# Kernel optimization log

Measured on AMD Instinct MI355X. Metric: run time of the kernel, lower is better.

The kernel has to match this reference:

```python
import jax, jax.numpy as jnp
import numpy as np

HIDDEN = 1024
NUM_HEADS = 16
HEAD_DIM = HIDDEN // NUM_HEADS


def setup_inputs() -> dict:
    key = jax.random.key(0)
    ks = jax.random.split(key, 11)
    s = 1.0 / np.sqrt(HIDDEN)
    x = jax.random.normal(ks[0], (4, 2048, HIDDEN), dtype=jnp.float32)
    Wq = jax.random.uniform(ks[1], (HIDDEN, HIDDEN), jnp.float32, -s, s)
    bq = jax.random.uniform(ks[2], (HIDDEN,), jnp.float32, -s, s)
    Wk = jax.random.uniform(ks[3], (HIDDEN, HIDDEN), jnp.float32, -s, s)
    bk = jax.random.uniform(ks[4], (HIDDEN,), jnp.float32, -s, s)
    Wv = jax.random.uniform(ks[5], (HIDDEN, HIDDEN), jnp.float32, -s, s)
    bv = jax.random.uniform(ks[6], (HIDDEN,), jnp.float32, -s, s)
    Wo = jax.random.uniform(ks[7], (HIDDEN, HIDDEN), jnp.float32, -s, s)
    bo = jax.random.uniform(ks[8], (HIDDEN,), jnp.float32, -s, s)
    ln_g = jnp.ones((HIDDEN,), jnp.float32)
    ln_b = jnp.zeros((HIDDEN,), jnp.float32)
    return {"x": x, "Wq": Wq, "bq": bq, "Wk": Wk, "bk": bk,
            "Wv": Wv, "bv": bv, "Wo": Wo, "bo": bo,
            "ln_g": ln_g, "ln_b": ln_b}


def _layer_norm(x, g, b, eps=1e-5):
    mu = jnp.mean(x, axis=-1, keepdims=True)
    var = jnp.var(x, axis=-1, keepdims=True)
    return (x - mu) * jax.lax.rsqrt(var + eps) * g + b


def reference(x, Wq, bq, Wk, bk, Wv, bv, Wo, bo, ln_g, ln_b):
    B, S, _ = x.shape
    residual = x
    h = _layer_norm(x, ln_g, ln_b)
    # projections (torch Linear: y = h @ W.T + b)
    q = (h @ Wq.T + bq).reshape(B, S, NUM_HEADS, HEAD_DIM).transpose(0, 2, 1, 3)
    k = (h @ Wk.T + bk).reshape(B, S, NUM_HEADS, HEAD_DIM).transpose(0, 2, 1, 3)
    v = (h @ Wv.T + bv).reshape(B, S, NUM_HEADS, HEAD_DIM).transpose(0, 2, 1, 3)
    scores = jnp.einsum('bhqd,bhkd->bhqk', q, k) / np.sqrt(HEAD_DIM).astype(np.float32)
    weights = jax.nn.softmax(scores, axis=-1)  # dropout = identity (eval mode)
    context = jnp.einsum('bhqk,bhkd->bhqd', weights, v)
    context = context.transpose(0, 2, 1, 3).reshape(B, S, HIDDEN)
    out = context @ Wo.T + bo
    return out + residual
```

## Files before the change

### kernel.cpp

```cpp
#include <hip/hip_runtime.h>

typedef unsigned short u16;
typedef unsigned int   u32;
using bf16x8 = __attribute__((ext_vector_type(8))) __bf16;
using f32x4  = __attribute__((ext_vector_type(4))) float;
using u32x2  = __attribute__((ext_vector_type(2))) unsigned int;

__device__ __forceinline__ u16 f2b(float f){
  union { float f; u32 i; } v; v.f = f;
  u32 r = v.i + 0x7FFFu + ((v.i >> 16) & 1u);
  return (u16)(r >> 16);
}
__device__ __forceinline__ u32 pk_bf16_trunc(float a, float b){
  return __builtin_amdgcn_perm(__float_as_uint(b), __float_as_uint(a), 0x07060302u);
}

__global__ __launch_bounds__(256) void cvt_w(const float* __restrict__ s0, const float* __restrict__ s1,
                                             const float* __restrict__ s2, const float* __restrict__ s3,
                                             u16* __restrict__ d){
  const float* srcs[4] = {s0, s1, s2, s3};
  const float* s = srcs[blockIdx.y];
  u16* dd = d + (size_t)blockIdx.y * (1024u * 1024u);
  const int i = (blockIdx.x * 256 + threadIdx.x) * 4;
  float4 v = *(const float4*)(s + i);
  uint2 o;
  o.x = (u32)f2b(v.x) | ((u32)f2b(v.y) << 16);
  o.y = (u32)f2b(v.z) | ((u32)f2b(v.w) << 16);
  *(uint2*)(dd + i) = o;
}

__global__ __launch_bounds__(256) void ln_kernel(const float* __restrict__ x, const float* __restrict__ g,
                                                 const float* __restrict__ be, u16* __restrict__ h){
  const int row = blockIdx.x, tid = threadIdx.x;
  const float* xr = x + (size_t)row * 1024u;
  float4 raw = *(const float4*)(xr + tid * 4);
  float s  = raw.x + raw.y + raw.z + raw.w;
  float sq = raw.x*raw.x + raw.y*raw.y + raw.z*raw.z + raw.w*raw.w;
  #pragma unroll
  for (int m = 1; m < 64; m <<= 1){ s += __shfl_xor(s, m); sq += __shfl_xor(sq, m); }
  __shared__ float ws[4], wq[4];
  if ((tid & 63) == 0){ ws[tid >> 6] = s; wq[tid >> 6] = sq; }
  __syncthreads();
  s  = ws[0] + ws[1] + ws[2] + ws[3];
  sq = wq[0] + wq[1] + wq[2] + wq[3];
  const float mu = s * (1.0f / 1024.0f);
  const float rstd = rsqrtf(sq * (1.0f / 1024.0f) - mu * mu + 1e-5f);
  float4 gg = *(const float4*)(g + tid * 4);
  float4 bb = *(const float4*)(be + tid * 4);
  float y0 = (raw.x - mu) * rstd * gg.x + bb.x;
  float y1 = (raw.y - mu) * rstd * gg.y + bb.y;
  float y2 = (raw.z - mu) * rstd * gg.z + bb.z;
  float y3 = (raw.w - mu) * rstd * gg.w + bb.w;
  uint2 outv;
  outv.x = (u32)f2b(y0) | ((u32)f2b(y1) << 16);
  outv.y = (u32)f2b(y2) | ((u32)f2b(y3) << 16);
  *(uint2*)(h + (size_t)row * 1024u + tid * 4) = outv;
}

__global__ __launch_bounds__(256) void gemm_qkv(const u16* __restrict__ A, const u16* __restrict__ Wcat,
                                                const float* __restrict__ bq, const float* __restrict__ bk,
                                                const float* __restrict__ bv,
                                                u16* __restrict__ qo, u16* __restrict__ ko, u16* __restrict__ vt){
  __shared__ u16 lA[2][4096];
  __shared__ u16 lB[2][4096];
  const int tid = threadIdx.x;
  const int lane = tid & 63, wv = tid >> 6, l15 = lane & 15, quad = lane >> 4;
  const int wr = wv >> 1, wc = wv & 1;
  const int row0 = blockIdx.x * 128, col0 = blockIdx.y * 128;
  const int K = 1024;

  const int r0_ = tid >> 2,         c0_ = tid & 3;
  const int r1_ = (256 + tid) >> 2, c1_ = (256 + tid) & 3;
  const u16* Asrc0 = A    + (size_t)(row0 + r0_) * K + (c0_ ^ ((r0_ >> 1) & 3)) * 8;
  const u16* Asrc1 = A    + (size_t)(row0 + r1_) * K + (c1_ ^ ((r1_ >> 1) & 3)) * 8;
  const u16* Bsrc0 = Wcat + (size_t)(col0 + r0_) * K + (c0_ ^ ((r0_ >> 1) & 3)) * 8;
  const u16* Bsrc1 = Wcat + (size_t)(col0 + r1_) * K + (c1_ ^ ((r1_ >> 1) & 3)) * 8;
  const int cr = (quad ^ ((l15 >> 1) & 3)) * 8;

  f32x4 acc[4][4] = {};
  uint4 ar0, ar1, br0, br1;
  ar0 = *(const uint4*)(Asrc0);
  ar1 = *(const uint4*)(Asrc1);
  br0 = *(const uint4*)(Bsrc0);
  br1 = *(const uint4*)(Bsrc1);
  *(uint4*)&lA[0][tid * 8] = ar0;
  *(uint4*)&lA[0][(256 + tid) * 8] = ar1;
  *(uint4*)&lB[0][tid * 8] = br0;
  *(uint4*)&lB[0][(256 + tid) * 8] = br1;
  ar0 = *(const uint4*)(Asrc0 + 32);
  ar1 = *(const uint4*)(Asrc1 + 32);
  br0 = *(const uint4*)(Bsrc0 + 32);
  br1 = *(const uint4*)(Bsrc1 + 32);
  __syncthreads();

  for (int kt = 0; kt < 32; ++kt){
    const int cur = kt & 1;
    if (kt < 31){
      *(uint4*)&lA[cur ^ 1][tid * 8] = ar0;
      *(uint4*)&lA[cur ^ 1][(256 + tid) * 8] = ar1;
      *(uint4*)&lB[cur ^ 1][tid * 8] = br0;
      *(uint4*)&lB[cur ^ 1][(256 + tid) * 8] = br1;
    }
    if (kt < 30){
      const int o = (kt + 2) * 32;
      ar0 = *(const uint4*)(Asrc0 + o);
      ar1 = *(const uint4*)(Asrc1 + o);
      br0 = *(const uint4*)(Bsrc0 + o);
      br1 = *(const uint4*)(Bsrc1 + o);
    }
    bf16x8 af[4], bf[4];
    #pragma unroll
    for (int i = 0; i < 4; ++i) af[i] = *(const bf16x8*)&lA[cur][(wr * 64 + i * 16 + l15) * 32 + cr];
    #pragma unroll
    for (int j = 0; j < 4; ++j) bf[j] = *(const bf16x8*)&lB[cur][(wc * 64 + j * 16 + l15) * 32 + cr];
    #pragma unroll
    for (int i = 0; i < 4; ++i)
      #pragma unroll
      for (int j = 0; j < 4; ++j)
        acc[i][j] = __builtin_amdgcn_mfma_f32_16x16x32_bf16(af[i], bf[j], acc[i][j], 0, 0, 0);
    __syncthreads();
  }
  const int sel = col0 >> 10;
  if (sel < 2){
    const float* bias = (sel == 0) ? bq : bk;
    u16* dst = (sel == 0) ? qo : ko;
    #pragma unroll
    for (int i = 0; i < 4; ++i){
      const int grow = row0 + wr * 64 + i * 16 + quad * 4;
      #pragma unroll
      for (int j = 0; j < 4; ++j){
        const int gcol = (col0 & 1023) + wc * 64 + j * 16 + l15;
        const float bb = bias[gcol];
        #pragma unroll
        for (int r = 0; r < 4; ++r){
          size_t off = (size_t)(grow + r) * 1024u + gcol;
          dst[off] = f2b(acc[i][j][r] + bb);
        }
      }
    }
  } else {
    u16* pw = &lA[0][0] + wv * 2048;
    const int bglob = row0 >> 11;
    const int head  = ((col0 & 1023) >> 6) + wc;
    const int srem0 = (row0 & 2047) + wr * 64;
    const size_t vbase = (size_t)((bglob * 16 + head) * 64) * 2048u;
    #pragma unroll
    for (int p = 0; p < 2; ++p){
      #pragma unroll
      for (int i2 = 0; i2 < 2; ++i2){
        const int i = p * 2 + i2;
        #pragma unroll
        for (int j = 0; j < 4; ++j){
          const int d = j * 16 + l15;
          const float bv_ = bv[(col0 & 1023) + wc * 64 + d];
          const int u = (i2 * 4 + quad) ^ (d & 7);
          uint2 pk;
          pk.x = (u32)f2b(acc[i][j][0] + bv_) | ((u32)f2b(acc[i][j][1] + bv_) << 16);
          pk.y = (u32)f2b(acc[i][j][2] + bv_) | ((u32)f2b(acc[i][j][3] + bv_) << 16);
          *(uint2*)&pw[d * 32 + u * 4] = pk;
        }
      }
      const int dl = lane;
      #pragma unroll
      for (int c = 0; c < 4; ++c){
        const int u0 = (2 * c) ^ (dl & 7), u1 = (2 * c + 1) ^ (dl & 7);
        uint2 lo = *(const uint2*)&pw[dl * 32 + u0 * 4];
        uint2 hi = *(const uint2*)&pw[dl * 32 + u1 * 4];
        uint4 o4; o4.x = lo.x; o4.y = lo.y; o4.z = hi.x; o4.w = hi.y;
        *(uint4*)(vt + vbase + (size_t)dl * 2048u + srem0 + p * 32 + c * 8) = o4;
      }
    }
  }
}

__global__ __launch_bounds__(256) void gemm_out(const u16* __restrict__ A, const u16* __restrict__ W,
                                                const float* __restrict__ bias, const float* __restrict__ res,
                                                float* __restrict__ C, int M, int N, int K){
  __shared__ u16 lA[2][4096];
  __shared__ u16 lB[2][4096];
  const int tid = threadIdx.x;
  const int lane = tid & 63, wv = tid >> 6, l15 = lane & 15, quad = lane >> 4;
  const int wr = wv >> 1, wc = wv & 1;
  const int row0 = blockIdx.x * 128, col0 = blockIdx.y * 128;

  const int r0_ = tid >> 2,         c0_ = tid & 3;
  const int r1_ = (256 + tid) >> 2, c1_ = (256 + tid) & 3;
  const u16* Asrc0 = A + (size_t)(row0 + r0_) * K + (c0_ ^ ((r0_ >> 1) & 3)) * 8;
  const u16* Asrc1 = A + (size_t)(row0 + r1_) * K + (c1_ ^ ((r1_ >> 1) & 3)) * 8;
  const u16* Bsrc0 = W + (size_t)(col0 + r0_) * K + (c0_ ^ ((r0_ >> 1) & 3)) * 8;
  const u16* Bsrc1 = W + (size_t)(col0 + r1_) * K + (c1_ ^ ((r1_ >> 1) & 3)) * 8;
  const int cr = (quad ^ ((l15 >> 1) & 3)) * 8;

  f32x4 acc[4][4] = {};
  const int nkt = K >> 5;
  uint4 ar0, ar1, br0, br1;
  ar0 = *(const uint4*)(Asrc0);
  ar1 = *(const uint4*)(Asrc1);
  br0 = *(const uint4*)(Bsrc0);
  br1 = *(const uint4*)(Bsrc1);
  *(uint4*)&lA[0][tid * 8] = ar0;
  *(uint4*)&lA[0][(256 + tid) * 8] = ar1;
  *(uint4*)&lB[0][tid * 8] = br0;
  *(uint4*)&lB[0][(256 + tid) * 8] = br1;
  ar0 = *(const uint4*)(Asrc0 + 32);
  ar1 = *(const uint4*)(Asrc1 + 32);
  br0 = *(const uint4*)(Bsrc0 + 32);
  br1 = *(const uint4*)(Bsrc1 + 32);
  __syncthreads();

  for (int kt = 0; kt < nkt; ++kt){
    const int cur = kt & 1;
    if (kt < nkt - 1){
      *(uint4*)&lA[cur ^ 1][tid * 8] = ar0;
      *(uint4*)&lA[cur ^ 1][(256 + tid) * 8] = ar1;
      *(uint4*)&lB[cur ^ 1][tid * 8] = br0;
      *(uint4*)&lB[cur ^ 1][(256 + tid) * 8] = br1;
    }
    if (kt < nkt - 2){
      const int o = (kt + 2) * 32;
      ar0 = *(const uint4*)(Asrc0 + o);
      ar1 = *(const uint4*)(Asrc1 + o);
      br0 = *(const uint4*)(Bsrc0 + o);
      br1 = *(const uint4*)(Bsrc1 + o);
    }
    bf16x8 af[4], bf[4];
    #pragma unroll
    for (int i = 0; i < 4; ++i) af[i] = *(const bf16x8*)&lA[cur][(wr * 64 + i * 16 + l15) * 32 + cr];
    #pragma unroll
    for (int j = 0; j < 4; ++j) bf[j] = *(const bf16x8*)&lB[cur][(wc * 64 + j * 16 + l15) * 32 + cr];
    #pragma unroll
    for (int i = 0; i < 4; ++i)
      #pragma unroll
      for (int j = 0; j < 4; ++j)
        acc[i][j] = __builtin_amdgcn_mfma_f32_16x16x32_bf16(af[i], bf[j], acc[i][j], 0, 0, 0);
    __syncthreads();
  }
  #pragma unroll
  for (int i = 0; i < 4; ++i){
    const int grow = row0 + wr * 64 + i * 16 + quad * 4;
    #pragma unroll
    for (int j = 0; j < 4; ++j){
      const int gcol = col0 + wc * 64 + j * 16 + l15;
      const float bb = bias[gcol];
      #pragma unroll
      for (int r = 0; r < 4; ++r){
        size_t off = (size_t)(grow + r) * N + gcol;
        C[off] = acc[i][j][r] + bb + res[off];
      }
    }
  }
}

__global__ __launch_bounds__(256, 2) void attn_kernel(const u16* __restrict__ Q, const u16* __restrict__ K,
                                                      const u16* __restrict__ Vt, u16* __restrict__ O){
  __shared__ u16 kls[2][64 * 64];
  __shared__ u16 vls[2][64 * 64];
  const int tid = threadIdx.x;
  const int lane = tid & 63, wv = tid >> 6, l15 = lane & 15, quad = lane >> 4;
  const int bh = blockIdx.x & 63, qt = blockIdx.x >> 6;
  const int b = bh >> 4, hh = bh & 15;
  const int q0 = qt * 256;
  const u16* Qg = Q + ((size_t)b * 2048u) * 1024u + hh * 64;
  const u16* Kg = K + ((size_t)b * 2048u) * 1024u + hh * 64;
  const u16* Vg = Vt + (size_t)bh * 64u * 2048u;
  u16* Og = O + ((size_t)b * 2048u) * 1024u + hh * 64;

  const int sr = tid >> 3, sc = tid & 7, sr2 = sr + 32;
  const int sx = (sc ^ (sr & 7)) * 8;
  const int c0 = ((quad ^ (l15 & 7))) * 8;

  const float QSCALE = 0.125f * 1.44269504f;
  bf16x8 qf2[4][2];
  #pragma unroll
  for (int g = 0; g < 4; ++g)
    #pragma unroll
    for (int kk = 0; kk < 2; ++kk){
      qf2[g][kk] = *(const bf16x8*)(Qg + (size_t)(q0 + wv * 64 + g * 16 + l15) * 1024u + kk * 32 + quad * 8);
      #pragma unroll
      for (int e = 0; e < 8; ++e) qf2[g][kk][e] = (__bf16)((float)qf2[g][kk][e] * QSCALE);
    }

  bf16x8 ones_f;
  {
    const __bf16 onev = (__bf16)1.0f, zerov = (__bf16)0.0f;
    #pragma unroll
    for (int e = 0; e < 8; ++e) ones_f[e] = (l15 == 0) ? onev : zerov;
  }

  f32x4 o2[4][4] = {};
  f32x4 o_l[4] = {};
  const f32x4 zf = {0.f, 0.f, 0.f, 0.f};

  uint4 kr0, kr1, vr0, vr1;
  kr0 = *(const uint4*)(Kg + (size_t)sr  * 1024u + sc * 8);
  vr0 = *(const uint4*)(Vg + (size_t)sr  * 2048u + sc * 8);
  kr1 = *(const uint4*)(Kg + (size_t)sr2 * 1024u + sc * 8);
  vr1 = *(const uint4*)(Vg + (size_t)sr2 * 2048u + sc * 8);
  *(uint4*)&kls[0][sr  * 64 + sx] = kr0;
  *(uint4*)&vls[0][sr  * 64 + sx] = vr0;
  *(uint4*)&kls[0][sr2 * 64 + sx] = kr1;
  *(uint4*)&vls[0][sr2 * 64 + sx] = vr1;
  kr0 = *(const uint4*)(Kg + (size_t)(64 + sr)  * 1024u + sc * 8);
  vr0 = *(const uint4*)(Vg + (size_t)sr  * 2048u + 64 + sc * 8);
  kr1 = *(const uint4*)(Kg + (size_t)(64 + sr2) * 1024u + sc * 8);
  vr1 = *(const uint4*)(Vg + (size_t)sr2 * 2048u + 64 + sc * 8);
  __syncthreads();

  for (int kt = 0; kt < 32; ++kt){
    const int cur = kt & 1;
    const u16* kb = kls[cur];
    const u16* vb = vls[cur];
    if (kt < 31){
      u16* kw = kls[cur ^ 1];
      u16* vw = vls[cur ^ 1];
      *(uint4*)&kw[sr  * 64 + sx] = kr0;
      *(uint4*)&vw[sr  * 64 + sx] = vr0;
      *(uint4*)&kw[sr2 * 64 + sx] = kr1;
      *(uint4*)&vw[sr2 * 64 + sx] = vr1;
    }
    if (kt < 30){
      const int s0 = (kt + 2) * 64;
      kr0 = *(const uint4*)(Kg + (size_t)(s0 + sr)  * 1024u + sc * 8);
      vr0 = *(const uint4*)(Vg + (size_t)sr  * 2048u + s0 + sc * 8);
      kr1 = *(const uint4*)(Kg + (size_t)(s0 + sr2) * 1024u + sc * 8);
      vr1 = *(const uint4*)(Vg + (size_t)sr2 * 2048u + s0 + sc * 8);
    }

    f32x4 s2[4][4];
    #pragma unroll
    for (int j = 0; j < 4; ++j){
      const int rb = (j * 16 + l15) * 64;
      bf16x8 kfr0 = *(const bf16x8*)&kb[rb + c0];
      bf16x8 kfr1 = *(const bf16x8*)&kb[rb + (c0 ^ 32)];
      #pragma unroll
      for (int g = 0; g < 4; ++g){
        f32x4 a = __builtin_amdgcn_mfma_f32_16x16x32_bf16(kfr0, qf2[g][0], zf, 0, 0, 0);
        s2[g][j] = __builtin_amdgcn_mfma_f32_16x16x32_bf16(kfr1, qf2[g][1], a, 0, 0, 0);
      }
    }

    #pragma unroll
    for (int g = 0; g < 4; ++g)
      #pragma unroll
      for (int j = 0; j < 4; ++j)
        #pragma unroll
        for (int r = 0; r < 4; ++r)
          s2[g][j][r] = __builtin_amdgcn_exp2f(s2[g][j][r]);

    #pragma unroll
    for (int kk = 0; kk < 2; ++kk){
      bf16x8 afr[4];
      #pragma unroll
      for (int g = 0; g < 4; ++g){
        const int j0 = kk * 2, j1 = j0 + 1;
        u32 A0 = pk_bf16_trunc(s2[g][j0][0], s2[g][j0][1]);
        u32 A1 = pk_bf16_trunc(s2[g][j0][2], s2[g][j0][3]);
        u32 B0 = pk_bf16_trunc(s2[g][j1][0], s2[g][j1][1]);
        u32 B1 = pk_bf16_trunc(s2[g][j1][2], s2[g][j1][3]);
        u32x2 r1 = __builtin_amdgcn_permlane32_swap(A0, B0, false, false);
        u32x2 r2 = __builtin_amdgcn_permlane16_swap(r1[0], r1[1], false, false);
        u32x2 r3 = __builtin_amdgcn_permlane32_swap(A1, B1, false, false);
        u32x2 r4 = __builtin_amdgcn_permlane16_swap(r3[0], r3[1], false, false);
        union { uint4 u; bf16x8 v; } cv;
        cv.u.x = r2[0]; cv.u.y = r4[0]; cv.u.z = r2[1]; cv.u.w = r4[1];
        afr[g] = cv.v;
      }
      #pragma unroll
      for (int g = 0; g < 4; ++g)
        o_l[g] = __builtin_amdgcn_mfma_f32_16x16x32_bf16(afr[g], ones_f, o_l[g], 0, 0, 0);
      #pragma unroll
      for (int j2 = 0; j2 < 4; ++j2){
        bf16x8 bfr = *(const bf16x8*)&vb[(j2 * 16 + l15) * 64 + (c0 ^ (kk * 32))];
        #pragma unroll
        for (int g = 0; g < 4; ++g)
          o2[g][j2] = __builtin_amdgcn_mfma_f32_16x16x32_bf16(afr[g], bfr, o2[g][j2], 0, 0, 0);
      }
    }
    __syncthreads();
  }

  #pragma unroll
  for (int g = 0; g < 4; ++g){
    float lr[4];
    #pragma unroll
    for (int r = 0; r < 4; ++r) lr[r] = 1.0f / __shfl(o_l[g][r], quad * 16);
    #pragma unroll
    for (int j2 = 0; j2 < 4; ++j2){
      #pragma unroll
      for (int r = 0; r < 4; ++r){
        const int qrow = q0 + wv * 64 + g * 16 + quad * 4 + r;
        const int d = j2 * 16 + l15;
        Og[(size_t)qrow * 1024u + d] = f2b(o2[g][j2][r] * lr[r]);
      }
    }
  }
}

extern "C" void kernel_launch(void* const* d_in, const int* in_sizes, int n_in,
                              void* d_out, int out_size, void* d_ws, size_t ws_size,
                              hipStream_t stream){
  (void)in_sizes; (void)n_in; (void)out_size; (void)ws_size;
  const float* x   = (const float*)d_in[0];
  const float* Wq  = (const float*)d_in[1];
  const float* bq  = (const float*)d_in[2];
  const float* Wk  = (const float*)d_in[3];
  const float* bk  = (const float*)d_in[4];
  const float* Wv  = (const float*)d_in[5];
  const float* bv  = (const float*)d_in[6];
  const float* Wo  = (const float*)d_in[7];
  const float* bo  = (const float*)d_in[8];
  const float* lng = (const float*)d_in[9];
  const float* lnb = (const float*)d_in[10];
  float* out = (float*)d_out;

  const size_t TE = (size_t)8192 * 1024;
  u16* ws0 = (u16*)d_ws;
  u16* ws1 = ws0 + TE;
  u16* ws2 = ws1 + TE;
  u16* wsw = ws2 + TE;
  u16* wob = wsw + (size_t)3 * 1024 * 1024;
  u16* vt  = (u16*)d_out;

  cvt_w<<<dim3(1024, 4), 256, 0, stream>>>(Wq, Wk, Wv, Wo, wsw);
  ln_kernel<<<dim3(8192), 256, 0, stream>>>(x, lng, lnb, ws0);
  gemm_qkv<<<dim3(64, 24), 256, 0, stream>>>(ws0, wsw, bq, bk, bv, ws1, ws2, vt);
  attn_kernel<<<dim3(512), 256, 0, stream>>>(ws1, ws2, vt, ws1);
  gemm_out<<<dim3(64, 8), 256, 0, stream>>>(ws1, wob, bo, x, out, 8192, 1024, 1024);
}
```

Before: 267.0 us.

## Use direct global-to-LDS loads in QKV and output projection GEMMs

Replaces the register-staged global loads and LDS stores in both GEMM kernels with global_load_lds direct-to-LDS transfers. Synchronisation becomes manual vmcnt/lgkmcnt waits plus raw s_barrier. The aim is to free VGPRs and cut the LDS store instructions from the main loop. The prefetch distance drops from two tiles (one in registers, one in LDS) to one. Correctness now depends on the hand-written waitcnt counts and on the 16-byte LDS layout matching lane order.

```diff
diff --git a/kernel.cpp b/kernel.cpp
--- a/kernel.cpp
+++ b/kernel.cpp
@@ -14,6 +14,10 @@
 __device__ __forceinline__ u32 pk_bf16_trunc(float a, float b){
   return __builtin_amdgcn_perm(__float_as_uint(b), __float_as_uint(a), 0x07060302u);
 }
+
+#define GLL(gp, lp) __builtin_amdgcn_global_load_lds( \
+    (const __attribute__((address_space(1))) void*)(gp), \
+    (__attribute__((address_space(3))) void*)(lp), 16, 0, 0)
 
 __global__ __launch_bounds__(256) void cvt_w(const float* __restrict__ s0, const float* __restrict__ s1,
                                              const float* __restrict__ s2, const float* __restrict__ s3,
@@ -78,36 +82,25 @@
   const int cr = (quad ^ ((l15 >> 1) & 3)) * 8;
 
   f32x4 acc[4][4] = {};
-  uint4 ar0, ar1, br0, br1;
-  ar0 = *(const uint4*)(Asrc0);
-  ar1 = *(const uint4*)(Asrc1);
-  br0 = *(const uint4*)(Bsrc0);
-  br1 = *(const uint4*)(Bsrc1);
-  *(uint4*)&lA[0][tid * 8] = ar0;
-  *(uint4*)&lA[0][(256 + tid) * 8] = ar1;
-  *(uint4*)&lB[0][tid * 8] = br0;
-  *(uint4*)&lB[0][(256 + tid) * 8] = br1;
-  ar0 = *(const uint4*)(Asrc0 + 32);
-  ar1 = *(const uint4*)(Asrc1 + 32);
-  br0 = *(const uint4*)(Bsrc0 + 32);
-  br1 = *(const uint4*)(Bsrc1 + 32);
-  __syncthreads();
+
+  GLL(Asrc0, &lA[0][tid * 8]);
+  GLL(Asrc1, &lA[0][(256 + tid) * 8]);
+  GLL(Bsrc0, &lB[0][tid * 8]);
+  GLL(Bsrc1, &lB[0][(256 + tid) * 8]);
 
   for (int kt = 0; kt < 32; ++kt){
     const int cur = kt & 1;
     if (kt < 31){
-      *(uint4*)&lA[cur ^ 1][tid * 8] = ar0;
-      *(uint4*)&lA[cur ^ 1][(256 + tid) * 8] = ar1;
-      *(uint4*)&lB[cur ^ 1][tid * 8] = br0;
-      *(uint4*)&lB[cur ^ 1][(256 + tid) * 8] = br1;
-    }
-    if (kt < 30){
-      const int o = (kt + 2) * 32;
-      ar0 = *(const uint4*)(Asrc0 + o);
-      ar1 = *(const uint4*)(Asrc1 + o);
-      br0 = *(const uint4*)(Bsrc0 + o);
-      br1 = *(const uint4*)(Bsrc1 + o);
-    }
+      const int o = (kt + 1) * 32;
+      GLL(Asrc0 + o, &lA[cur ^ 1][tid * 8]);
+      GLL(Asrc1 + o, &lA[cur ^ 1][(256 + tid) * 8]);
+      GLL(Bsrc0 + o, &lB[cur ^ 1][tid * 8]);
+      GLL(Bsrc1 + o, &lB[cur ^ 1][(256 + tid) * 8]);
+      asm volatile("s_waitcnt vmcnt(4)" ::: "memory");
+    } else {
+      asm volatile("s_waitcnt vmcnt(0)" ::: "memory");
+    }
+    asm volatile("s_barrier" ::: "memory");
     bf16x8 af[4], bf[4];
     #pragma unroll
     for (int i = 0; i < 4; ++i) af[i] = *(const bf16x8*)&lA[cur][(wr * 64 + i * 16 + l15) * 32 + cr];
@@ -118,8 +111,11 @@
       #pragma unroll
       for (int j = 0; j < 4; ++j)
         acc[i][j] = __builtin_amdgcn_mfma_f32_16x16x32_bf16(af[i], bf[j], acc[i][j], 0, 0, 0);
-    __syncthreads();
-  }
+    asm volatile("s_waitcnt lgkmcnt(0)" ::: "memory");
+    __builtin_amdgcn_sched_barrier(0);
+    asm volatile("s_barrier" ::: "memory");
+  }
+
   const int sel = col0 >> 10;
   if (sel < 2){
     const float* bias = (sel == 0) ? bq : bk;
@@ -193,36 +189,25 @@
 
   f32x4 acc[4][4] = {};
   const int nkt = K >> 5;
-  uint4 ar0, ar1, br0, br1;
-  ar0 = *(const uint4*)(Asrc0);
-  ar1 = *(const uint4*)(Asrc1);
-  br0 = *(const uint4*)(Bsrc0);
-  br1 = *(const uint4*)(Bsrc1);
-  *(uint4*)&lA[0][tid * 8] = ar0;
-  *(uint4*)&lA[0][(256 + tid) * 8] = ar1;
-  *(uint4*)&lB[0][tid * 8] = br0;
-  *(uint4*)&lB[0][(256 + tid) * 8] = br1;
-  ar0 = *(const uint4*)(Asrc0 + 32);
-  ar1 = *(const uint4*)(Asrc1 + 32);
-  br0 = *(const uint4*)(Bsrc0 + 32);
-  br1 = *(const uint4*)(Bsrc1 + 32);
-  __syncthreads();
+
+  GLL(Asrc0, &lA[0][tid * 8]);
+  GLL(Asrc1, &lA[0][(256 + tid) * 8]);
+  GLL(Bsrc0, &lB[0][tid * 8]);
+  GLL(Bsrc1, &lB[0][(256 + tid) * 8]);
 
   for (int kt = 0; kt < nkt; ++kt){
     const int cur = kt & 1;
     if (kt < nkt - 1){
-      *(uint4*)&lA[cur ^ 1][tid * 8] = ar0;
-      *(uint4*)&lA[cur ^ 1][(256 + tid) * 8] = ar1;
-      *(uint4*)&lB[cur ^ 1][tid * 8] = br0;
-      *(uint4*)&lB[cur ^ 1][(256 + tid) * 8] = br1;
-    }
-    if (kt < nkt - 2){
-      const int o = (kt + 2) * 32;
-      ar0 = *(const uint4*)(Asrc0 + o);
-      ar1 = *(const uint4*)(Asrc1 + o);
-      br0 = *(const uint4*)(Bsrc0 + o);
-      br1 = *(const uint4*)(Bsrc1 + o);
-    }
+      const int o = (kt + 1) * 32;
+      GLL(Asrc0 + o, &lA[cur ^ 1][tid * 8]);
+      GLL(Asrc1 + o, &lA[cur ^ 1][(256 + tid) * 8]);
+      GLL(Bsrc0 + o, &lB[cur ^ 1][tid * 8]);
+      GLL(Bsrc1 + o, &lB[cur ^ 1][(256 + tid) * 8]);
+      asm volatile("s_waitcnt vmcnt(4)" ::: "memory");
+    } else {
+      asm volatile("s_waitcnt vmcnt(0)" ::: "memory");
+    }
+    asm volatile("s_barrier" ::: "memory");
     bf16x8 af[4], bf[4];
     #pragma unroll
     for (int i = 0; i < 4; ++i) af[i] = *(const bf16x8*)&lA[cur][(wr * 64 + i * 16 + l15) * 32 + cr];
@@ -233,7 +218,9 @@
       #pragma unroll
       for (int j = 0; j < 4; ++j)
         acc[i][j] = __builtin_amdgcn_mfma_f32_16x16x32_bf16(af[i], bf[j], acc[i][j], 0, 0, 0);
-    __syncthreads();
+    asm volatile("s_waitcnt lgkmcnt(0)" ::: "memory");
+    __builtin_amdgcn_sched_barrier(0);
+    asm volatile("s_barrier" ::: "memory");
   }
   #pragma unroll
   for (int i = 0; i < 4; ++i){
```

Result: slower. 290.8 us (+8.9%).

## Merge weight conversion into layernorm kernel and compute softmax denominators with VALU

Applied to the files above, without the earlier changes.

Folds the weight bf16 conversion into the layernorm launch as extra blocks, removing one kernel launch. In attention, drops the extra MFMA against a ones vector that produced row sums. Instead each lane accumulates truncated-bf16 exp values in registers and reduces them with cross-lane shuffles at the end. This removes 8 MFMAs per iteration at the cost of extra VALU adds and some shuffles. Truncating to bf16 before summing keeps the denominator consistent with the P values fed to the PV MFMA.

```diff
diff --git a/kernel.cpp b/kernel.cpp
--- a/kernel.cpp
+++ b/kernel.cpp
@@ -15,23 +15,26 @@
   return __builtin_amdgcn_perm(__float_as_uint(b), __float_as_uint(a), 0x07060302u);
 }
 
-__global__ __launch_bounds__(256) void cvt_w(const float* __restrict__ s0, const float* __restrict__ s1,
-                                             const float* __restrict__ s2, const float* __restrict__ s3,
-                                             u16* __restrict__ d){
-  const float* srcs[4] = {s0, s1, s2, s3};
-  const float* s = srcs[blockIdx.y];
-  u16* dd = d + (size_t)blockIdx.y * (1024u * 1024u);
-  const int i = (blockIdx.x * 256 + threadIdx.x) * 4;
-  float4 v = *(const float4*)(s + i);
-  uint2 o;
-  o.x = (u32)f2b(v.x) | ((u32)f2b(v.y) << 16);
-  o.y = (u32)f2b(v.z) | ((u32)f2b(v.w) << 16);
-  *(uint2*)(dd + i) = o;
-}
-
-__global__ __launch_bounds__(256) void ln_kernel(const float* __restrict__ x, const float* __restrict__ g,
-                                                 const float* __restrict__ be, u16* __restrict__ h){
-  const int row = blockIdx.x, tid = threadIdx.x;
+__global__ __launch_bounds__(256) void pre_kernel(const float* __restrict__ x, const float* __restrict__ g,
+                                                  const float* __restrict__ be, u16* __restrict__ h,
+                                                  const float* __restrict__ s0, const float* __restrict__ s1,
+                                                  const float* __restrict__ s2, const float* __restrict__ s3,
+                                                  u16* __restrict__ wd){
+  const int tid = threadIdx.x;
+  if (blockIdx.x >= 8192){
+    const int b2 = blockIdx.x - 8192;
+    const float* srcs[4] = {s0, s1, s2, s3};
+    const float* s = srcs[b2 >> 10];
+    u16* dd = wd + (size_t)(b2 >> 10) * (1024u * 1024u);
+    const int i = ((b2 & 1023) * 256 + tid) * 4;
+    float4 v = *(const float4*)(s + i);
+    uint2 o;
+    o.x = (u32)f2b(v.x) | ((u32)f2b(v.y) << 16);
+    o.y = (u32)f2b(v.z) | ((u32)f2b(v.w) << 16);
+    *(uint2*)(dd + i) = o;
+    return;
+  }
+  const int row = blockIdx.x;
   const float* xr = x + (size_t)row * 1024u;
   float4 raw = *(const float4*)(xr + tid * 4);
   float s  = raw.x + raw.y + raw.z + raw.w;
@@ -280,15 +283,8 @@
       for (int e = 0; e < 8; ++e) qf2[g][kk][e] = (__bf16)((float)qf2[g][kk][e] * QSCALE);
     }
 
-  bf16x8 ones_f;
-  {
-    const __bf16 onev = (__bf16)1.0f, zerov = (__bf16)0.0f;
-    #pragma unroll
-    for (int e = 0; e < 8; ++e) ones_f[e] = (l15 == 0) ? onev : zerov;
-  }
-
   f32x4 o2[4][4] = {};
-  f32x4 o_l[4] = {};
+  float dl[4] = {0.f, 0.f, 0.f, 0.f};
   const f32x4 zf = {0.f, 0.f, 0.f, 0.f};
 
   uint4 kr0, kr1, vr0, vr1;
@@ -340,12 +336,18 @@
     }
 
     #pragma unroll
-    for (int g = 0; g < 4; ++g)
+    for (int g = 0; g < 4; ++g){
+      float t = 0.f;
       #pragma unroll
       for (int j = 0; j < 4; ++j)
         #pragma unroll
-        for (int r = 0; r < 4; ++r)
-          s2[g][j][r] = __builtin_amdgcn_exp2f(s2[g][j][r]);
+        for (int r = 0; r < 4; ++r){
+          float p = __builtin_amdgcn_exp2f(s2[g][j][r]);
+          s2[g][j][r] = p;
+          t += __uint_as_float(__float_as_uint(p) & 0xFFFF0000u);
+        }
+      dl[g] += t;
+    }
 
     #pragma unroll
     for (int kk = 0; kk < 2; ++kk){
@@ -366,9 +368,6 @@
         afr[g] = cv.v;
       }
       #pragma unroll
-      for (int g = 0; g < 4; ++g)
-        o_l[g] = __builtin_amdgcn_mfma_f32_16x16x32_bf16(afr[g], ones_f, o_l[g], 0, 0, 0);
-      #pragma unroll
       for (int j2 = 0; j2 < 4; ++j2){
         bf16x8 bfr = *(const bf16x8*)&vb[(j2 * 16 + l15) * 64 + (c0 ^ (kk * 32))];
         #pragma unroll
@@ -381,9 +380,15 @@
 
   #pragma unroll
   for (int g = 0; g < 4; ++g){
+    dl[g] += __shfl_xor(dl[g], 16);
+    dl[g] += __shfl_xor(dl[g], 32);
+  }
+
+  #pragma unroll
+  for (int g = 0; g < 4; ++g){
     float lr[4];
     #pragma unroll
-    for (int r = 0; r < 4; ++r) lr[r] = 1.0f / __shfl(o_l[g][r], quad * 16);
+    for (int r = 0; r < 4; ++r) lr[r] = 1.0f / __shfl(dl[g], quad * 4 + r);
     #pragma unroll
     for (int j2 = 0; j2 < 4; ++j2){
       #pragma unroll
@@ -421,8 +426,7 @@
   u16* wob = wsw + (size_t)3 * 1024 * 1024;
   u16* vt  = (u16*)d_out;
 
-  cvt_w<<<dim3(1024, 4), 256, 0, stream>>>(Wq, Wk, Wv, Wo, wsw);
-  ln_kernel<<<dim3(8192), 256, 0, stream>>>(x, lng, lnb, ws0);
+  pre_kernel<<<dim3(12288), 256, 0, stream>>>(x, lng, lnb, ws0, Wq, Wk, Wv, Wo, wsw);
   gemm_qkv<<<dim3(64, 24), 256, 0, stream>>>(ws0, wsw, bq, bk, bv, ws1, ws2, vt);
   attn_kernel<<<dim3(512), 256, 0, stream>>>(ws1, ws2, vt, ws1);
   gemm_out<<<dim3(64, 8), 256, 0, stream>>>(ws1, wob, bo, x, out, 8192, 1024, 1024);
```

Result: slower. 280.5 us (+5.0%).

## Load GEMM B fragments directly to registers, fuse weight conversion into layernorm

Applied to the files above, without the earlier changes.

Both GEMMs stop staging the weight tile through LDS. Each wave now loads its B fragments straight from global memory into registers, double-buffered across a 2x unrolled K loop, and launch bounds request 4 blocks per CU. The weight bf16 conversion and layernorm are merged into one launch to save a kernel launch. The change cuts LDS traffic and footprint, at the cost of redundant global loads of B across waves that share a column tile, with more register pressure and cache reliance.

```diff
diff --git a/kernel.cpp b/kernel.cpp
--- a/kernel.cpp
+++ b/kernel.cpp
@@ -15,23 +15,26 @@
   return __builtin_amdgcn_perm(__float_as_uint(b), __float_as_uint(a), 0x07060302u);
 }
 
-__global__ __launch_bounds__(256) void cvt_w(const float* __restrict__ s0, const float* __restrict__ s1,
-                                             const float* __restrict__ s2, const float* __restrict__ s3,
-                                             u16* __restrict__ d){
-  const float* srcs[4] = {s0, s1, s2, s3};
-  const float* s = srcs[blockIdx.y];
-  u16* dd = d + (size_t)blockIdx.y * (1024u * 1024u);
-  const int i = (blockIdx.x * 256 + threadIdx.x) * 4;
-  float4 v = *(const float4*)(s + i);
-  uint2 o;
-  o.x = (u32)f2b(v.x) | ((u32)f2b(v.y) << 16);
-  o.y = (u32)f2b(v.z) | ((u32)f2b(v.w) << 16);
-  *(uint2*)(dd + i) = o;
-}
-
-__global__ __launch_bounds__(256) void ln_kernel(const float* __restrict__ x, const float* __restrict__ g,
-                                                 const float* __restrict__ be, u16* __restrict__ h){
-  const int row = blockIdx.x, tid = threadIdx.x;
+__global__ __launch_bounds__(256) void pre_kernel(const float* __restrict__ x, const float* __restrict__ g,
+                                                  const float* __restrict__ be, u16* __restrict__ h,
+                                                  const float* __restrict__ s0, const float* __restrict__ s1,
+                                                  const float* __restrict__ s2, const float* __restrict__ s3,
+                                                  u16* __restrict__ wd){
+  const int tid = threadIdx.x;
+  if (blockIdx.x >= 8192){
+    const int b2 = blockIdx.x - 8192;
+    const float* srcs[4] = {s0, s1, s2, s3};
+    const float* s = srcs[b2 >> 10];
+    u16* dd = wd + (size_t)(b2 >> 10) * (1024u * 1024u);
+    const int i = ((b2 & 1023) * 256 + tid) * 4;
+    float4 v = *(const float4*)(s + i);
+    uint2 o;
+    o.x = (u32)f2b(v.x) | ((u32)f2b(v.y) << 16);
+    o.y = (u32)f2b(v.z) | ((u32)f2b(v.w) << 16);
+    *(uint2*)(dd + i) = o;
+    return;
+  }
+  const int row = blockIdx.x;
   const float* xr = x + (size_t)row * 1024u;
   float4 raw = *(const float4*)(xr + tid * 4);
   float s  = raw.x + raw.y + raw.z + raw.w;
@@ -57,12 +60,11 @@
   *(uint2*)(h + (size_t)row * 1024u + tid * 4) = outv;
 }
 
-__global__ __launch_bounds__(256) void gemm_qkv(const u16* __restrict__ A, const u16* __restrict__ Wcat,
-                                                const float* __restrict__ bq, const float* __restrict__ bk,
-                                                const float* __restrict__ bv,
-                                                u16* __restrict__ qo, u16* __restrict__ ko, u16* __restrict__ vt){
+__global__ __launch_bounds__(256, 4) void gemm_qkv(const u16* __restrict__ A, const u16* __restrict__ Wcat,
+                                                   const float* __restrict__ bq, const float* __restrict__ bk,
+                                                   const float* __restrict__ bv,
+                                                   u16* __restrict__ qo, u16* __restrict__ ko, u16* __restrict__ vt){
   __shared__ u16 lA[2][4096];
-  __shared__ u16 lB[2][4096];
   const int tid = threadIdx.x;
   const int lane = tid & 63, wv = tid >> 6, l15 = lane & 15, quad = lane >> 4;
   const int wr = wv >> 1, wc = wv & 1;
@@ -71,55 +73,62 @@
 
   const int r0_ = tid >> 2,         c0_ = tid & 3;
   const int r1_ = (256 + tid) >> 2, c1_ = (256 + tid) & 3;
-  const u16* Asrc0 = A    + (size_t)(row0 + r0_) * K + (c0_ ^ ((r0_ >> 1) & 3)) * 8;
-  const u16* Asrc1 = A    + (size_t)(row0 + r1_) * K + (c1_ ^ ((r1_ >> 1) & 3)) * 8;
-  const u16* Bsrc0 = Wcat + (size_t)(col0 + r0_) * K + (c0_ ^ ((r0_ >> 1) & 3)) * 8;
-  const u16* Bsrc1 = Wcat + (size_t)(col0 + r1_) * K + (c1_ ^ ((r1_ >> 1) & 3)) * 8;
+  const u16* Asrc0 = A + (size_t)(row0 + r0_) * K + (c0_ ^ ((r0_ >> 1) & 3)) * 8;
+  const u16* Asrc1 = A + (size_t)(row0 + r1_) * K + (c1_ ^ ((r1_ >> 1) & 3)) * 8;
   const int cr = (quad ^ ((l15 >> 1) & 3)) * 8;
+  const u16* Bf = Wcat + (size_t)(col0 + wc * 64 + l15) * 1024u + quad * 8;
 
   f32x4 acc[4][4] = {};
-  uint4 ar0, ar1, br0, br1;
+  uint4 ar0, ar1;
+  bf16x8 bc0, bc1, bc2, bc3, bn0, bn1, bn2, bn3;
+
   ar0 = *(const uint4*)(Asrc0);
   ar1 = *(const uint4*)(Asrc1);
-  br0 = *(const uint4*)(Bsrc0);
-  br1 = *(const uint4*)(Bsrc1);
   *(uint4*)&lA[0][tid * 8] = ar0;
   *(uint4*)&lA[0][(256 + tid) * 8] = ar1;
-  *(uint4*)&lB[0][tid * 8] = br0;
-  *(uint4*)&lB[0][(256 + tid) * 8] = br1;
   ar0 = *(const uint4*)(Asrc0 + 32);
   ar1 = *(const uint4*)(Asrc1 + 32);
-  br0 = *(const uint4*)(Bsrc0 + 32);
-  br1 = *(const uint4*)(Bsrc1 + 32);
+  bc0 = *(const bf16x8*)(Bf);
+  bc1 = *(const bf16x8*)(Bf + 16384);
+  bc2 = *(const bf16x8*)(Bf + 32768);
+  bc3 = *(const bf16x8*)(Bf + 49152);
   __syncthreads();
 
-  for (int kt = 0; kt < 32; ++kt){
-    const int cur = kt & 1;
-    if (kt < 31){
-      *(uint4*)&lA[cur ^ 1][tid * 8] = ar0;
-      *(uint4*)&lA[cur ^ 1][(256 + tid) * 8] = ar1;
-      *(uint4*)&lB[cur ^ 1][tid * 8] = br0;
-      *(uint4*)&lB[cur ^ 1][(256 + tid) * 8] = br1;
-    }
-    if (kt < 30){
-      const int o = (kt + 2) * 32;
-      ar0 = *(const uint4*)(Asrc0 + o);
-      ar1 = *(const uint4*)(Asrc1 + o);
-      br0 = *(const uint4*)(Bsrc0 + o);
-      br1 = *(const uint4*)(Bsrc1 + o);
-    }
-    bf16x8 af[4], bf[4];
-    #pragma unroll
-    for (int i = 0; i < 4; ++i) af[i] = *(const bf16x8*)&lA[cur][(wr * 64 + i * 16 + l15) * 32 + cr];
-    #pragma unroll
-    for (int j = 0; j < 4; ++j) bf[j] = *(const bf16x8*)&lB[cur][(wc * 64 + j * 16 + l15) * 32 + cr];
-    #pragma unroll
-    for (int i = 0; i < 4; ++i)
-      #pragma unroll
-      for (int j = 0; j < 4; ++j)
-        acc[i][j] = __builtin_amdgcn_mfma_f32_16x16x32_bf16(af[i], bf[j], acc[i][j], 0, 0, 0);
-    __syncthreads();
-  }
+#define QKV_BODY(KT, C0, C1, C2, C3, N0, N1, N2, N3) { \
+    const int cur = (KT) & 1; \
+    if ((KT) < 31){ \
+      *(uint4*)&lA[cur ^ 1][tid * 8] = ar0; \
+      *(uint4*)&lA[cur ^ 1][(256 + tid) * 8] = ar1; \
+    } \
+    if ((KT) < 30){ \
+      ar0 = *(const uint4*)(Asrc0 + ((KT) + 2) * 32); \
+      ar1 = *(const uint4*)(Asrc1 + ((KT) + 2) * 32); \
+    } \
+    if ((KT) < 31){ \
+      N0 = *(const bf16x8*)(Bf +         ((KT) + 1) * 32); \
+      N1 = *(const bf16x8*)(Bf + 16384 + ((KT) + 1) * 32); \
+      N2 = *(const bf16x8*)(Bf + 32768 + ((KT) + 1) * 32); \
+      N3 = *(const bf16x8*)(Bf + 49152 + ((KT) + 1) * 32); \
+    } \
+    bf16x8 af[4]; \
+    _Pragma("unroll") \
+    for (int i = 0; i < 4; ++i) af[i] = *(const bf16x8*)&lA[cur][(wr * 64 + i * 16 + l15) * 32 + cr]; \
+    _Pragma("unroll") \
+    for (int i = 0; i < 4; ++i){ \
+      acc[i][0] = __builtin_amdgcn_mfma_f32_16x16x32_bf16(af[i], C0, acc[i][0], 0, 0, 0); \
+      acc[i][1] = __builtin_amdgcn_mfma_f32_16x16x32_bf16(af[i], C1, acc[i][1], 0, 0, 0); \
+      acc[i][2] = __builtin_amdgcn_mfma_f32_16x16x32_bf16(af[i], C2, acc[i][2], 0, 0, 0); \
+      acc[i][3] = __builtin_amdgcn_mfma_f32_16x16x32_bf16(af[i], C3, acc[i][3], 0, 0, 0); \
+    } \
+    __syncthreads(); \
+  }
+
+  for (int kt2 = 0; kt2 < 32; kt2 += 2){
+    QKV_BODY(kt2,     bc0, bc1, bc2, bc3, bn0, bn1, bn2, bn3);
+    QKV_BODY(kt2 + 1, bn0, bn1, bn2, bn3, bc0, bc1, bc2, bc3);
+  }
+#undef QKV_BODY
+
   const int sel = col0 >> 10;
   if (sel < 2){
     const float* bias = (sel == 0) ? bq : bk;
@@ -173,11 +182,10 @@
   }
 }
 
-__global__ __launch_bounds__(256) void gemm_out(const u16* __restrict__ A, const u16* __restrict__ W,
-                                                const float* __restrict__ bias, const float* __restrict__ res,
-                                                float* __restrict__ C, int M, int N, int K){
+__global__ __launch_bounds__(256, 4) void gemm_out(const u16* __restrict__ A, const u16* __restrict__ W,
+                                                   const float* __restrict__ bias, const float* __restrict__ res,
+                                                   float* __restrict__ C, int M, int N, int K){
   __shared__ u16 lA[2][4096];
-  __shared__ u16 lB[2][4096];
   const int tid = threadIdx.x;
   const int lane = tid & 63, wv = tid >> 6, l15 = lane & 15, quad = lane >> 4;
   const int wr = wv >> 1, wc = wv & 1;
@@ -187,54 +195,62 @@
   const int r1_ = (256 + tid) >> 2, c1_ = (256 + tid) & 3;
   const u16* Asrc0 = A + (size_t)(row0 + r0_) * K + (c0_ ^ ((r0_ >> 1) & 3)) * 8;
   const u16* Asrc1 = A + (size_t)(row0 + r1_) * K + (c1_ ^ ((r1_ >> 1) & 3)) * 8;
-  const u16* Bsrc0 = W + (size_t)(col0 + r0_) * K + (c0_ ^ ((r0_ >> 1) & 3)) * 8;
-  const u16* Bsrc1 = W + (size_t)(col0 + r1_) * K + (c1_ ^ ((r1_ >> 1) & 3)) * 8;
   const int cr = (quad ^ ((l15 >> 1) & 3)) * 8;
+  const size_t j16K = (size_t)16 * K;
+  const u16* Bf = W + (size_t)(col0 + wc * 64 + l15) * K + quad * 8;
 
   f32x4 acc[4][4] = {};
   const int nkt = K >> 5;
-  uint4 ar0, ar1, br0, br1;
+  uint4 ar0, ar1;
+  bf16x8 bc0, bc1, bc2, bc3, bn0, bn1, bn2, bn3;
+
   ar0 = *(const uint4*)(Asrc0);
   ar1 = *(const uint4*)(Asrc1);
-  br0 = *(const uint4*)(Bsrc0);
-  br1 = *(const uint4*)(Bsrc1);
   *(uint4*)&lA[0][tid * 8] = ar0;
   *(uint4*)&lA[0][(256 + tid) * 8] = ar1;
-  *(uint4*)&lB[0][tid * 8] = br0;
-  *(uint4*)&lB[0][(256 + tid) * 8] = br1;
   ar0 = *(const uint4*)(Asrc0 + 32);
   ar1 = *(const uint4*)(Asrc1 + 32);
-  br0 = *(const uint4*)(Bsrc0 + 32);
-  br1 = *(const uint4*)(Bsrc1 + 32);
+  bc0 = *(const bf16x8*)(Bf);
+  bc1 = *(const bf16x8*)(Bf + j16K);
+  bc2 = *(const bf16x8*)(Bf + 2 * j16K);
+  bc3 = *(const bf16x8*)(Bf + 3 * j16K);
   __syncthreads();
 
-  for (int kt = 0; kt < nkt; ++kt){
-    const int cur = kt & 1;
-    if (kt < nkt - 1){
-      *(uint4*)&lA[cur ^ 1][tid * 8] = ar0;
-      *(uint4*)&lA[cur ^ 1][(256 + tid) * 8] = ar1;
-      *(uint4*)&lB[cur ^ 1][tid * 8] = br0;
-      *(uint4*)&lB[cur ^ 1][(256 + tid) * 8] = br1;
-    }
-    if (kt < nkt - 2){
-      const int o = (kt + 2) * 32;
-      ar0 = *(const uint4*)(Asrc0 + o);
-      ar1 = *(const uint4*)(Asrc1 + o);
-      br0 = *(const uint4*)(Bsrc0 + o);
-      br1 = *(const uint4*)(Bsrc1 + o);
-    }
-    bf16x8 af[4], bf[4];
-    #pragma unroll
-    for (int i = 0; i < 4; ++i) af[i] = *(const bf16x8*)&lA[cur][(wr * 64 + i * 16 + l15) * 32 + cr];
-    #pragma unroll
-    for (int j = 0; j < 4; ++j) bf[j] = *(const bf16x8*)&lB[cur][(wc * 64 + j * 16 + l15) * 32 + cr];
-    #pragma unroll
-    for (int i = 0; i < 4; ++i)
-      #pragma unroll
-      for (int j = 0; j < 4; ++j)
-        acc[i][j] = __builtin_amdgcn_mfma_f32_16x16x32_bf16(af[i], bf[j], acc[i][j], 0, 0, 0);
-    __syncthreads();
-  }
+#define OUT_BODY(KT, C0, C1, C2, C3, N0, N1, N2, N3) { \
+    const int cur = (KT) & 1; \
+    if ((KT) < nkt - 1){ \
+      *(uint4*)&lA[cur ^ 1][tid * 8] = ar0; \
+      *(uint4*)&lA[cur ^ 1][(256 + tid) * 8] = ar1; \
+    } \
+    if ((KT) < nkt - 2){ \
+      ar0 = *(const uint4*)(Asrc0 + ((KT) + 2) * 32); \
+      ar1 = *(const uint4*)(Asrc1 + ((KT) + 2) * 32); \
+    } \
+    if ((KT) < nkt - 1){ \
+      N0 = *(const bf16x8*)(Bf +            ((KT) + 1) * 32); \
+      N1 = *(const bf16x8*)(Bf + j16K     + ((KT) + 1) * 32); \
+      N2 = *(const bf16x8*)(Bf + 2 * j16K + ((KT) + 1) * 32); \
+      N3 = *(const bf16x8*)(Bf + 3 * j16K + ((KT) + 1) * 32); \
+    } \
+    bf16x8 af[4]; \
+    _Pragma("unroll") \
+    for (int i = 0; i < 4; ++i) af[i] = *(const bf16x8*)&lA[cur][(wr * 64 + i * 16 + l15) * 32 + cr]; \
+    _Pragma("unroll") \
+    for (int i = 0; i < 4; ++i){ \
+      acc[i][0] = __builtin_amdgcn_mfma_f32_16x16x32_bf16(af[i], C0, acc[i][0], 0, 0, 0); \
+      acc[i][1] = __builtin_amdgcn_mfma_f32_16x16x32_bf16(af[i], C1, acc[i][1], 0, 0, 0); \
+      acc[i][2] = __builtin_amdgcn_mfma_f32_16x16x32_bf16(af[i], C2, acc[i][2], 0, 0, 0); \
+      acc[i][3] = __builtin_amdgcn_mfma_f32_16x16x32_bf16(af[i], C3, acc[i][3], 0, 0, 0); \
+    } \
+    __syncthreads(); \
+  }
+
+  for (int kt2 = 0; kt2 < nkt; kt2 += 2){
+    OUT_BODY(kt2,     bc0, bc1, bc2, bc3, bn0, bn1, bn2, bn3);
+    OUT_BODY(kt2 + 1, bn0, bn1, bn2, bn3, bc0, bc1, bc2, bc3);
+  }
+#undef OUT_BODY
+
   #pragma unroll
   for (int i = 0; i < 4; ++i){
     const int grow = row0 + wr * 64 + i * 16 + quad * 4;
@@ -421,8 +437,7 @@
   u16* wob = wsw + (size_t)3 * 1024 * 1024;
   u16* vt  = (u16*)d_out;
 
-  cvt_w<<<dim3(1024, 4), 256, 0, stream>>>(Wq, Wk, Wv, Wo, wsw);
-  ln_kernel<<<dim3(8192), 256, 0, stream>>>(x, lng, lnb, ws0);
+  pre_kernel<<<dim3(12288), 256, 0, stream>>>(x, lng, lnb, ws0, Wq, Wk, Wv, Wo, wsw);
   gemm_qkv<<<dim3(64, 24), 256, 0, stream>>>(ws0, wsw, bq, bk, bv, ws1, ws2, vt);
   attn_kernel<<<dim3(512), 256, 0, stream>>>(ws1, ws2, vt, ws1);
   gemm_out<<<dim3(64, 8), 256, 0, stream>>>(ws1, wob, bo, x, out, 8192, 1024, 1024);
```

New measurement: 323.8 us. 1.21x slower.
